# Kernel tuning notes

Hardware: AMD Instinct MI355X
Metric: run time of the kernel (lower is better)

The kernel has to match this reference:

```python
import jax, jax.numpy as jnp
import numpy as np
from jax import lax

B, DZ, H, U, T, V = 256, 512, 512, 16, 16, 512  # batch, latent, lstm hidden, segments, steps/segment, vocab


def setup_inputs() -> dict:
    key = jax.random.key(0)
    ks = jax.random.split(key, 32)
    w = lambda k, shape: jax.random.normal(k, shape, jnp.float32) * 0.05
    d = {
        'z': jax.random.normal(ks[0], (B, DZ), jnp.float32),
        'x': jax.random.randint(ks[1], (B, U * T), 0, V),
        # conductor init-state projection: DZ -> 4H
        'Wc': w(ks[2], (4 * H, DZ)), 'bc': jnp.zeros((4 * H,), jnp.float32),
        # conductor 2-layer LSTM (input H, hidden H)
        'cWih0': w(ks[3], (4 * H, H)), 'cWhh0': w(ks[4], (4 * H, H)),
        'cbih0': jnp.zeros((4 * H,), jnp.float32), 'cbhh0': jnp.zeros((4 * H,), jnp.float32),
        'cWih1': w(ks[5], (4 * H, H)), 'cWhh1': w(ks[6], (4 * H, H)),
        'cbih1': jnp.zeros((4 * H,), jnp.float32), 'cbhh1': jnp.zeros((4 * H,), jnp.float32),
        # decoder init-state projection: H -> 4H
        'Wd': w(ks[7], (4 * H, H)), 'bd': jnp.zeros((4 * H,), jnp.float32),
        # decoder 2-layer LSTM (layer0 input 2H, layer1 input H, hidden H)
        'dWih0': w(ks[8], (4 * H, 2 * H)), 'dWhh0': w(ks[9], (4 * H, H)),
        'dbih0': jnp.zeros((4 * H,), jnp.float32), 'dbhh0': jnp.zeros((4 * H,), jnp.float32),
        'dWih1': w(ks[10], (4 * H, H)), 'dWhh1': w(ks[11], (4 * H, H)),
        'dbih1': jnp.zeros((4 * H,), jnp.float32), 'dbhh1': jnp.zeros((4 * H,), jnp.float32),
        # token embedding and output distribution head
        'emb': w(ks[12], (V, H)),
        'Wo': w(ks[13], (V, H)), 'bo': jnp.zeros((V,), jnp.float32),
    }
    return d


def _cell(x, h, c, Wih, Whh, bih, bhh):
    # PyTorch LSTM gate order: i, f, g, o
    g = x @ Wih.T + bih + h @ Whh.T + bhh
    i, f, gg, o = jnp.split(g, 4, axis=-1)
    c = jax.nn.sigmoid(f) * c + jax.nn.sigmoid(i) * jnp.tanh(gg)
    h = jax.nn.sigmoid(o) * jnp.tanh(c)
    return h, c


def _lstm_layer(xp, h0, c0, Whh, bhh):
    # xp: [N, T, 4H] = precomputed x @ Wih.T + bih
    def step(carry, xg):
        h, c = carry
        g = xg + h @ Whh.T + bhh
        i, f, gg, o = jnp.split(g, 4, axis=-1)
        c = jax.nn.sigmoid(f) * c + jax.nn.sigmoid(i) * jnp.tanh(gg)
        h = jax.nn.sigmoid(o) * jnp.tanh(c)
        return (h, c), h
    _, ys = lax.scan(step, (h0, c0), jnp.swapaxes(xp, 0, 1))
    return jnp.swapaxes(ys, 0, 1)  # [N, T, H]


def reference(z, x, Wc, bc, cWih0, cWhh0, cbih0, cbhh0, cWih1, cWhh1, cbih1, cbhh1,
              Wd, bd, dWih0, dWhh0, dbih0, dbhh0, dWih1, dWhh1, dbih1, dbhh1,
              emb, Wo, bo):
    Bz = z.shape[0]
    # --- conductor ---
    ci = jnp.tanh(z @ Wc.T + bc)  # [B, 4H]
    h1, h2, c1, c2 = ci[:, :H], ci[:, H:2 * H], ci[:, 2 * H:3 * H], ci[:, 3 * H:]
    o0 = jnp.zeros((Bz, H), ci.dtype)

    def cstep(carry, _):
        o, h1, c1, h2, c2 = carry
        h1, c1 = _cell(o, h1, c1, cWih0, cWhh0, cbih0, cbhh0)
        h2, c2 = _cell(h1, h2, c2, cWih1, cWhh1, cbih1, cbhh1)
        return (h2, h1, c1, h2, c2), h2

    _, couts = lax.scan(cstep, (o0, h1, c1, h2, c2), None, length=U)
    cond_out = jnp.swapaxes(couts, 0, 1)  # [B, U, H]

    # --- decoder init states ---
    states = jnp.tanh(cond_out @ Wd.T + bd).reshape(Bz * U, 4 * H)
    dh1, dh2, dc1, dc2 = (states[:, :H], states[:, H:2 * H],
                          states[:, 2 * H:3 * H], states[:, 3 * H:])
    h_init = dh1 + dh2  # [BU, H]

    # --- teacher-forced decoder ---
    xt = x.reshape(Bz * U, T)
    e = emb[xt]  # [BU, T, H]
    e = jnp.concatenate([jnp.zeros((Bz * U, 1, H), e.dtype), e[:, :-1]], axis=1)
    inp = jnp.concatenate(
        [e, jnp.broadcast_to(h_init[:, None], (Bz * U, T, H))], axis=-1)  # [BU, T, 2H]

    y0 = _lstm_layer(inp @ dWih0.T + dbih0, dh1, dc1, dWhh0, dbhh0)
    y1 = _lstm_layer(y0 @ dWih1.T + dbih1, dh2, dc2, dWhh1, dbhh1)
    dist = jax.nn.softmax(y1 @ Wo.T + bo, axis=-1)  # [BU, T, V]
    return dist.reshape(Bz, U * T, V)
```

## Files before the change

kernel.cpp:

```cpp
#include <hip/hip_runtime.h>
#include <math.h>

#define AS1 __attribute__((address_space(1)))
#define AS3 __attribute__((address_space(3)))

typedef __attribute__((ext_vector_type(8))) short short8v;
typedef __attribute__((ext_vector_type(16))) float f32x16;

constexpr size_t PA4c = (size_t)4096 * 512;
constexpr size_t PABc = (size_t)256 * 512;

__device__ __forceinline__ float sigmoidf_(float x) { return 1.f / (1.f + expf(-x)); }
__device__ __forceinline__ unsigned int f2bfu(float f) {
    unsigned int u = __float_as_uint(f);
    return (u + 0x7FFF + ((u >> 16) & 1)) >> 16;
}
__device__ __forceinline__ float bf2f(unsigned int s) { return __uint_as_float(s << 16); }
__device__ __forceinline__ unsigned int pack2(float v) {
    unsigned int b0 = f2bfu(v);
    unsigned int b1 = f2bfu(v - bf2f(b0));
    return b0 | (b1 << 16);
}
__device__ __forceinline__ float unpack2(unsigned int p) { return bf2f(p & 0xffffu) + bf2f(p >> 16); }

__device__ __forceinline__ void xswz(int d, int ngx, int ngy, int& bx, int& by) {
    int nwg = ngx * ngy;
    int q = nwg >> 3, r = nwg & 7, xcd = d & 7, pos = d >> 3;
    int logical = (xcd < r ? xcd * (q + 1) : r * (q + 1) + (xcd - r) * q) + pos;
    bx = logical % ngx; by = logical / ngx;
}

template<int FM, int FN>
__device__ __forceinline__ void gemm_core(
    const short* __restrict__ A1, const short* __restrict__ B1,
    const short* __restrict__ A2, const short* __restrict__ B2,
    int M, int N, int nsteps, int pairSwitch,
    int bx, int by, short* lds, f32x16 (&acc)[FM][FN])
{
    constexpr int ABLK = 4 * FM, BBLK = 2 * FN;
    constexpr int ACH = 2 * ABLK * 2, BCH = 2 * BBLK * 2;
    constexpr int CHT = ACH + BCH;
    constexpr int CPW = CHT / 8;
    constexpr int NBUF = 3;
    constexpr int BUFSH = CHT * 512;
    const int tid = threadIdx.x, lane = tid & 63, wid = tid >> 6;
    const int wm = wid >> 1, wn = wid & 1;
    const int l31 = lane & 31, loct = lane >> 5;
    const int mblk0 = by * ABLK, nblk0 = bx * BBLK;
    const size_t planeA = (size_t)M * 512, planeB = (size_t)N * 512;

    const short* cur[CPW];
    const short* nxt[CPW];
    int ldo[CPW];
    #pragma unroll
    for (int i = 0; i < CPW; ++i) {
        int c = wid * CPW + i;
        ldo[i] = c * 512;
        size_t off;
        const short *b1, *b2;
        if (c < ACH) {
            int plane = c / (ABLK * 2), rem = c % (ABLK * 2), blk = rem >> 1, piece = rem & 1;
            off = (size_t)plane * planeA + (size_t)(mblk0 + blk) * 16384 + piece * 512 + lane * 8;
            b1 = A1; b2 = A2;
        } else {
            int cb = c - ACH;
            int plane = cb / (BBLK * 2), rem = cb % (BBLK * 2), blk = rem >> 1, piece = rem & 1;
            off = (size_t)plane * planeB + (size_t)(nblk0 + blk) * 16384 + piece * 512 + lane * 8;
            b1 = B1; b2 = B2;
        }
        cur[i] = b1 + off;
        nxt[i] = b2 ? (b2 + off) : (b1 + off);
    }

    #pragma unroll
    for (int fm = 0; fm < FM; ++fm)
        #pragma unroll
        for (int fn = 0; fn < FN; ++fn)
            acc[fm][fn] = (f32x16){};

    auto STAGE = [&](int bufIdx) {
        short* db = lds + bufIdx * BUFSH;
        #pragma unroll
        for (int i = 0; i < CPW; ++i) {
            __builtin_amdgcn_global_load_lds((const AS1 unsigned int*)cur[i],
                                             (AS3 unsigned int*)(db + ldo[i]), 16, 0, 0);
            cur[i] += 1024;
        }
    };

    STAGE(0); STAGE(1);
    asm volatile("s_waitcnt vmcnt(%0)" :: "n"(CPW) : "memory");
    __builtin_amdgcn_s_barrier();

    for (int t = 0; t < nsteps; ++t) {
        int s = t + NBUF - 1;
        if (s < nsteps) {
            if (s == pairSwitch) {
                #pragma unroll
                for (int i = 0; i < CPW; ++i) cur[i] = nxt[i];
            }
            STAGE(s % NBUF);
        }
        const short* L = lds + (t % NBUF) * BUFSH;
        #pragma unroll
        for (int ksub = 0; ksub < 2; ++ksub) {
            short8v a[FM][2], b[FN][2];
            #pragma unroll
            for (int p = 0; p < 2; ++p) {
                #pragma unroll
                for (int f = 0; f < FM; ++f)
                    a[f][p] = *(const short8v*)(L + (p * (ABLK * 2) + (wm * FM + f) * 2 + ksub) * 512
                                                  + loct * 256 + l31 * 8);
                #pragma unroll
                for (int f = 0; f < FN; ++f)
                    b[f][p] = *(const short8v*)(L + (ACH + p * (BBLK * 2) + (wn * FN + f) * 2 + ksub) * 512
                                                  + loct * 256 + l31 * 8);
            }
            #pragma unroll
            for (int pp = 0; pp < 3; ++pp) {
                const int pa = (pp == 2) ? 1 : 0, pb = (pp == 1) ? 1 : 0;
                #pragma unroll
                for (int fm = 0; fm < FM; ++fm)
                    #pragma unroll
                    for (int fn = 0; fn < FN; ++fn)
                        acc[fm][fn] = __builtin_amdgcn_mfma_f32_32x32x16_bf16(
                            a[fm][pa], b[fn][pb], acc[fm][fn], 0, 0, 0);
            }
        }
        if (t + 2 < nsteps)
            asm volatile("s_waitcnt vmcnt(%0) lgkmcnt(0)" :: "n"(CPW) : "memory");
        else
            asm volatile("s_waitcnt vmcnt(0) lgkmcnt(0)" ::: "memory");
        __builtin_amdgcn_s_barrier();
    }
}

template<int FM, int FN>
__device__ __forceinline__ void epi_f32(f32x16 (&acc)[FM][FN], int bx, int by, int N,
                                        float* __restrict__ Cout, const float* __restrict__ bias, int act)
{
    constexpr int ROWS = 128 * FM, COLS = 64 * FN;
    const int tid = threadIdx.x, lane = tid & 63, wid = tid >> 6;
    const int wm = wid >> 1, wn = wid & 1, l31 = lane & 31, loct = lane >> 5;
    #pragma unroll
    for (int fm = 0; fm < FM; ++fm)
        #pragma unroll
        for (int fn = 0; fn < FN; ++fn) {
            int col = bx * COLS + wn * FN * 32 + fn * 32 + l31;
            int rb  = by * ROWS + wm * FM * 32 + fm * 32 + 4 * loct;
            #pragma unroll
            for (int reg = 0; reg < 16; ++reg) {
                int row = rb + (reg & 3) + 8 * (reg >> 2);
                float xv = acc[fm][fn][reg] + (bias ? bias[row] : 0.f);
                if (act) xv = tanhf(xv);
                Cout[(size_t)row * N + col] = xv;
            }
        }
}

template<int FM, int FN>
__device__ __forceinline__ void epi_pack(f32x16 (&acc)[FM][FN], int bx, int by, int N,
                                         unsigned int* __restrict__ packOut)
{
    constexpr int ROWS = 128 * FM, COLS = 64 * FN;
    const int tid = threadIdx.x, lane = tid & 63, wid = tid >> 6;
    const int wm = wid >> 1, wn = wid & 1, l31 = lane & 31, loct = lane >> 5;
    uint4* P4 = (uint4*)packOut;
    #pragma unroll
    for (int fm = 0; fm < FM; ++fm)
        #pragma unroll
        for (int fn = 0; fn < FN; ++fn) {
            int col = bx * COLS + wn * FN * 32 + fn * 32 + l31;
            int ub = by * (ROWS / 4) + wm * FM * 8 + fm * 8 + loct;
            #pragma unroll
            for (int ug = 0; ug < 4; ++ug) {
                int u = ub + 2 * ug;
                uint4 v;
                v.x = pack2(acc[fm][fn][4 * ug + 0]);
                v.y = pack2(acc[fm][fn][4 * ug + 1]);
                v.z = pack2(acc[fm][fn][4 * ug + 2]);
                v.w = pack2(acc[fm][fn][4 * ug + 3]);
                P4[(size_t)u * N + col] = v;
            }
        }
}

template<int FM, int FN>
__device__ __forceinline__ void epi_gate(
    f32x16 (&acc)[FM][FN], int bx, int by, int N,
    short* lds, const float* __restrict__ bab,
    const unsigned int* __restrict__ hgP,
    const unsigned int* __restrict__ embT,
    const int* __restrict__ xidx,
    float* __restrict__ cT,
    short* __restrict__ hout, size_t hps,
    short* __restrict__ condp, size_t cps, int ustep)
{
    constexpr int ABLK = 4 * FM, BBLK = 2 * FN;
    constexpr int ROWS = 32 * ABLK, COLS = 32 * BBLK;
    constexpr int CHN = ABLK * BBLK * 256;
    const int tid = threadIdx.x, lane = tid & 63, wid = tid >> 6;
    const int wm = wid >> 1, wn = wid & 1, l31 = lane & 31, loct = lane >> 5;
    short* hl = lds;
    #pragma unroll
    for (int fm = 0; fm < FM; ++fm) {
        #pragma unroll
        for (int fn = 0; fn < FN; ++fn) {
            const int col = bx * COLS + wn * FN * 32 + fn * 32 + l31;
            const int tok = xidx ? xidx[(size_t)col * 16] : -1;
            const int ub = by * (ROWS / 4) + wm * FM * 8 + fm * 8 + loct;
            #pragma unroll
            for (int ug = 0; ug < 4; ++ug) {
                int u = ub + 2 * ug;
                float gi = acc[fm][fn][4 * ug + 0];
                float gf = acc[fm][fn][4 * ug + 1];
                float gg = acc[fm][fn][4 * ug + 2];
                float go = acc[fm][fn][4 * ug + 3];
                float4 bv = *(const float4*)&bab[4 * u];
                gi += bv.x; gf += bv.y; gg += bv.z; go += bv.w;
                if (hgP) {
                    uint4 hv = ((const uint4*)hgP)[(size_t)u * N + col];
                    gi += unpack2(hv.x); gf += unpack2(hv.y);
                    gg += unpack2(hv.z); go += unpack2(hv.w);
                }
                if (embT && tok >= 0) {
                    uint4 ev = ((const uint4*)embT)[(size_t)u * 512 + tok];
                    gi += unpack2(ev.x); gf += unpack2(ev.y);
                    gg += unpack2(ev.z); go += unpack2(ev.w);
                }
                size_t cidx = (size_t)u * N + col;
                float c = sigmoidf_(gf) * cT[cidx] + sigmoidf_(gi) * tanhf(gg);
                cT[cidx] = c;
                float h = sigmoidf_(go) * tanhf(c);
                unsigned int p01 = pack2(h);
                int u_loc = wm * FM * 8 + fm * 8 + loct + 2 * ug;
                int m_loc = wn * FN * 32 + fn * 32 + l31;
                int offl = ((m_loc >> 5) * ABLK + (u_loc >> 3)) * 256 + (m_loc & 31) * 8 + (u_loc & 7);
                hl[offl] = (short)(p01 & 0xffffu);
                hl[CHN + offl] = (short)(p01 >> 16);
                if (condp) {
                    int np = col * 16 + ustep;
                    size_t offc = ((size_t)((np >> 5) * 64 + (u >> 3))) * 256 + (np & 31) * 8 + (u & 7);
                    condp[offc] = (short)(p01 & 0xffffu);
                    condp[cps + offc] = (short)(p01 >> 16);
                }
            }
        }
    }
    __syncthreads();
    constexpr int LB = (ABLK == 8) ? 3 : 2;
    for (int p = 0; p < 2; ++p) {
        for (int jj = tid; jj < CHN / 8; jj += 512) {
            int lc = jj >> 5, m31 = jj & 31;
            int m5 = lc >> LB, u3 = lc & (ABLK - 1);
            size_t gc = (size_t)((bx * BBLK + m5) * 64 + by * ABLK + u3);
            *(short8v*)(hout + p * hps + gc * 256 + m31 * 8) = *(const short8v*)(hl + p * CHN + jj * 8);
        }
    }
}

template<int FM, int FN>
__global__ __launch_bounds__(512, 1) void gemm_f32k(
    const short* A1, const short* B1, const short* A2, const short* B2,
    int M, int N, int nsteps, int psw,
    float* Cout, const float* bias, int act)
{
    __shared__ __align__(16) short lds[3 * (2 * (4 * FM) * 2 + 2 * (2 * FN) * 2) * 512];
    int d = blockIdx.y * gridDim.x + blockIdx.x;
    int bx, by; xswz(d, gridDim.x, gridDim.y, bx, by);
    f32x16 acc[FM][FN];
    gemm_core<FM, FN>(A1, B1, A2, B2, M, N, nsteps, psw, bx, by, lds, acc);
    epi_f32<FM, FN>(acc, bx, by, N, Cout, bias, act);
}

template<int FM, int FN>
__global__ __launch_bounds__(512, 1) void gemm_packk(
    const short* A1, const short* B1, const short* A2, const short* B2,
    int M, int N, int nsteps, int psw, unsigned int* packOut)
{
    __shared__ __align__(16) short lds[3 * (2 * (4 * FM) * 2 + 2 * (2 * FN) * 2) * 512];
    int d = blockIdx.y * gridDim.x + blockIdx.x;
    int bx, by; xswz(d, gridDim.x, gridDim.y, bx, by);
    f32x16 acc[FM][FN];
    gemm_core<FM, FN>(A1, B1, A2, B2, M, N, nsteps, psw, bx, by, lds, acc);
    epi_pack<FM, FN>(acc, bx, by, N, packOut);
}

__device__ __forceinline__ void gbar(unsigned int* bar, unsigned int target)
{
    __syncthreads();
    if (threadIdx.x == 0) {
        __hip_atomic_fetch_add(bar, 1u, __ATOMIC_ACQ_REL, __HIP_MEMORY_SCOPE_AGENT);
        while (__hip_atomic_load(bar, __ATOMIC_ACQUIRE, __HIP_MEMORY_SCOPE_AGENT) < target)
            __builtin_amdgcn_s_sleep(2);
    }
    __syncthreads();
}

__global__ __launch_bounds__(512, 1) void cond_lstm(
    const short* cWih0P, const short* cWhh0P, const short* cWih1P, const short* cWhh1P,
    const float* babc0, const float* babc1,
    float* c1T, float* c2T,
    short* h1p0, short* h1p1, short* h2p0, short* h2p1,
    short* condp, unsigned int* bar)
{
    __shared__ __align__(16) short lds[3 * 12288];
    const int d = blockIdx.x;
    const int xcd = d & 7, j = d >> 3;
    const int by = xcd * 2 + (j & 1), bx = j >> 1;
    unsigned int gen = 0;
    for (int u = 0; u < 16; ++u) {
        const int pin = u & 1;
        short* h1in  = pin ? h1p1 : h1p0;  short* h1out = pin ? h1p0 : h1p1;
        short* h2in  = pin ? h2p1 : h2p0;  short* h2out = pin ? h2p0 : h2p1;
        {
            f32x16 acc[1][1];
            if (u == 0)
                gemm_core<1, 1>(cWhh0P, h1in, nullptr, nullptr, 2048, 256, 16, 100, bx, by, lds, acc);
            else
                gemm_core<1, 1>(cWih0P, h2in, cWhh0P, h1in, 2048, 256, 32, 16, bx, by, lds, acc);
            epi_gate<1, 1>(acc, bx, by, 256, lds, babc0, nullptr, nullptr, nullptr,
                           c1T, h1out, PABc, nullptr, 0, 0);
        }
        gbar(bar, (++gen) * 64);
        {
            f32x16 acc[1][1];
            gemm_core<1, 1>(cWih1P, h1out, cWhh1P, h2in, 2048, 256, 32, 16, bx, by, lds, acc);
            epi_gate<1, 1>(acc, bx, by, 256, lds, babc1, nullptr, nullptr, nullptr,
                           c2T, h2out, PABc, condp, PA4c, u);
        }
        gbar(bar, (++gen) * 64);
    }
}

__global__ __launch_bounds__(512, 1) void dec_k1(
    int doGate,
    const short* Ag, const short* Bg, const float* bab,
    const unsigned int* hgP, const unsigned int* embT, const int* xidx,
    float* cT, short* hout,
    const short* Aw, const short* Bw, float* Lout)
{
    __shared__ __align__(16) short lds[3 * 24576];
    const int dd = blockIdx.x;
    if (doGate) {
        int bx, by; xswz(dd, 32, 8, bx, by);
        f32x16 acc[2][2];
        gemm_core<2, 2>(Ag, Bg, nullptr, nullptr, 2048, 4096, 16, 100, bx, by, lds, acc);
        epi_gate<2, 2>(acc, bx, by, 4096, lds, bab, hgP, embT, xidx, cT, hout, PA4c, nullptr, 0, 0);
        __syncthreads();
    }
    if (Aw) {
        int bx, by; xswz(dd, 64, 4, bx, by);
        f32x16 acc[1][1];
        gemm_core<1, 1>(Aw, Bw, nullptr, nullptr, 512, 4096, 16, 100, bx, by, lds, acc);
        epi_f32<1, 1>(acc, bx, by, 4096, Lout, nullptr, 0);
    }
}

__global__ __launch_bounds__(512, 1) void dec_k2(
    int doGate,
    const short* A1, const short* B1, const short* A2, const short* B2,
    const float* bab, float* cT, short* hout,
    const float* Lsrc, const float* bo, float* outp, int tstep)
{
    __shared__ __align__(16) short lds[3 * 24576];
    const int dd = blockIdx.x;
    if (doGate) {
        int bx, by; xswz(dd, 32, 8, bx, by);
        f32x16 acc[2][2];
        gemm_core<2, 2>(A1, B1, A2, B2, 2048, 4096, 32, 16, bx, by, lds, acc);
        epi_gate<2, 2>(acc, bx, by, 4096, lds, bab, nullptr, nullptr, nullptr, cT, hout, PA4c, nullptr, 0, 0);
        __syncthreads();
    }
    if (Lsrc) {
        float* tile = (float*)lds;
        float* red  = (float*)lds + 16 * 513;
        float* red2 = red + 512;
        const int tid = threadIdx.x;
        const int mj = tid & 15, vs = tid >> 4;
        const int m = dd * 16 + mj;
        float mx = -1e30f;
        for (int i = 0; i < 16; ++i) {
            int v = vs * 16 + i;
            mx = fmaxf(mx, Lsrc[(size_t)v * 4096 + m] + bo[v]);
        }
        red[vs * 16 + mj] = mx;
        __syncthreads();
        for (int o = 16; o >= 1; o >>= 1) {
            if (vs < o) red[vs * 16 + mj] = fmaxf(red[vs * 16 + mj], red[(vs + o) * 16 + mj]);
            __syncthreads();
        }
        mx = red[mj];
        float sum = 0.f;
        for (int i = 0; i < 16; ++i) {
            int v = vs * 16 + i;
            float e = expf(Lsrc[(size_t)v * 4096 + m] + bo[v] - mx);
            sum += e;
            tile[mj * 513 + v] = e;
        }
        red2[vs * 16 + mj] = sum;
        __syncthreads();
        for (int o = 16; o >= 1; o >>= 1) {
            if (vs < o) red2[vs * 16 + mj] += red2[(vs + o) * 16 + mj];
            __syncthreads();
        }
        const int r = tid >> 5, c = tid & 31;
        float invr = 1.f / red2[r];
        for (int k = 0; k < 16; ++k) {
            int v = k * 32 + c;
            outp[((size_t)(dd * 16 + r) * 16 + tstep) * 512 + v] = tile[r * 513 + v] * invr;
        }
    }
}

struct PrepEnt { const float* src; const float* src2; void* dst; int ldw, col0, perm, total, op; };
struct PrepArgs { PrepEnt e[18]; int n; };

__global__ void prep_all(PrepArgs pa)
{
    for (int ei = 0; ei < pa.n; ++ei) {
        PrepEnt E = pa.e[ei];
        for (int o = blockIdx.x * 256 + threadIdx.x; o < E.total; o += gridDim.x * 256) {
            if (E.op == 0) {
                int c = o >> 8, w = o & 255, r = w >> 3, jj = w & 7;
                int n = (c >> 6) * 32 + r, k = (c & 63) * 8 + jj;
                int nsrc = E.perm ? ((n >> 2) + 512 * (n & 3)) : n;
                float v = E.src[(size_t)nsrc * E.ldw + E.col0 + k];
                unsigned int b0 = f2bfu(v);
                short* pl = (short*)E.dst;
                pl[o] = (short)b0;
                pl[E.total + o] = (short)f2bfu(v - bf2f(b0));
            } else {
                int src = (o >> 2) + 512 * (o & 3);
                ((float*)E.dst)[o] = E.src[src] + E.src2[src];
            }
        }
    }
}

__global__ void split_ci(const float* __restrict__ ciT, short* __restrict__ h1, short* __restrict__ h2,
                         size_t ps, float* __restrict__ c1T, float* __restrict__ c2T)
{
    int idx = blockIdx.x * 256 + threadIdx.x;
    int u = idx >> 8, b = idx & 255;
    float v1 = ciT[(size_t)u * 256 + b];
    float v2 = ciT[(size_t)(512 + u) * 256 + b];
    c1T[(size_t)u * 256 + b] = ciT[(size_t)(1024 + u) * 256 + b];
    c2T[(size_t)u * 256 + b] = ciT[(size_t)(1536 + u) * 256 + b];
    size_t o = ((size_t)((b >> 5) * 64 + (u >> 3))) * 256 + (b & 31) * 8 + (u & 7);
    unsigned int p;
    p = f2bfu(v1); h1[o] = (short)p; h1[ps + o] = (short)f2bfu(v1 - bf2f(p));
    p = f2bfu(v2); h2[o] = (short)p; h2[ps + o] = (short)f2bfu(v2 - bf2f(p));
}

__global__ void split_states(const float* __restrict__ GT, short* __restrict__ h0, short* __restrict__ h1d,
                             size_t ps, float* __restrict__ c0T, float* __restrict__ c1dT)
{
    int idx = blockIdx.x * 256 + threadIdx.x;
    int u = idx >> 12, m = idx & 4095;
    float a = GT[(size_t)u * 4096 + m];
    float b = GT[(size_t)(512 + u) * 4096 + m];
    c0T[(size_t)u * 4096 + m]  = GT[(size_t)(1024 + u) * 4096 + m];
    c1dT[(size_t)u * 4096 + m] = GT[(size_t)(1536 + u) * 4096 + m];
    size_t o = ((size_t)((m >> 5) * 64 + (u >> 3))) * 256 + (m & 31) * 8 + (u & 7);
    unsigned int p;
    p = f2bfu(a); h0[o] = (short)p; h0[ps + o] = (short)f2bfu(a - bf2f(p));
    p = f2bfu(b); h1d[o] = (short)p; h1d[ps + o] = (short)f2bfu(b - bf2f(p));
}

extern "C" void kernel_launch(void* const* d_in, const int* in_sizes, int n_in,
                              void* d_out, int out_size, void* d_ws, size_t ws_size,
                              hipStream_t stream)
{
    const float* z     = (const float*)d_in[0];
    const int*   x     = (const int*)  d_in[1];
    const float* Wc    = (const float*)d_in[2];
    const float* bc    = (const float*)d_in[3];
    const float* cWih0 = (const float*)d_in[4];
    const float* cWhh0 = (const float*)d_in[5];
    const float* cbih0 = (const float*)d_in[6];
    const float* cbhh0 = (const float*)d_in[7];
    const float* cWih1 = (const float*)d_in[8];
    const float* cWhh1 = (const float*)d_in[9];
    const float* cbih1 = (const float*)d_in[10];
    const float* cbhh1 = (const float*)d_in[11];
    const float* Wd    = (const float*)d_in[12];
    const float* bd    = (const float*)d_in[13];
    const float* dWih0 = (const float*)d_in[14];
    const float* dWhh0 = (const float*)d_in[15];
    const float* dbih0 = (const float*)d_in[16];
    const float* dbhh0 = (const float*)d_in[17];
    const float* dWih1 = (const float*)d_in[18];
    const float* dWhh1 = (const float*)d_in[19];
    const float* dbih1 = (const float*)d_in[20];
    const float* dbhh1 = (const float*)d_in[21];
    const float* emb   = (const float*)d_in[22];
    const float* Wo    = (const float*)d_in[23];
    const float* bo    = (const float*)d_in[24];
    float* out = (float*)d_out;
    (void)in_sizes; (void)n_in; (void)out_size; (void)ws_size;

    char* wsb = (char*)d_ws;
    size_t off = 0;
    auto alloc = [&](size_t bytes) -> void* {
        off = (off + 255) & ~(size_t)255;
        void* p = wsb + off;
        off += bytes;
        return p;
    };
    const size_t PW  = (size_t)2048 * 512;
    const size_t PWo = (size_t)512 * 512;

    short* WcP    = (short*)alloc(2 * PW * 2);
    short* WdP    = (short*)alloc(2 * PW * 2);
    short* dW1P   = (short*)alloc(2 * PW * 2);
    short* dW2P   = (short*)alloc(2 * PW * 2);
    short* cWih0P = (short*)alloc(2 * PW * 2);
    short* cWhh0P = (short*)alloc(2 * PW * 2);
    short* cWih1P = (short*)alloc(2 * PW * 2);
    short* cWhh1P = (short*)alloc(2 * PW * 2);
    short* dWhh0P = (short*)alloc(2 * PW * 2);
    short* dWih1P = (short*)alloc(2 * PW * 2);
    short* dWhh1P = (short*)alloc(2 * PW * 2);
    short* WoP    = (short*)alloc(2 * PWo * 2);
    short* zpl    = (short*)alloc(2 * PABc * 2);
    short* embpl  = (short*)alloc(2 * PWo * 2);
    float* babc0  = (float*)alloc(2048 * 4);
    float* babc1  = (float*)alloc(2048 * 4);
    float* babd0  = (float*)alloc(2048 * 4);
    float* babd1  = (float*)alloc(2048 * 4);
    float* GbufT  = (float*)alloc((size_t)2048 * 4096 * 4);
    unsigned int* hinitgP = (unsigned int*)alloc((size_t)512 * 4096 * 4 * 4);
    unsigned int* embW0P  = (unsigned int*)alloc((size_t)512 * 512 * 4 * 4);
    short* h1pl0 = (short*)alloc(2 * PABc * 2);
    short* h1pl1 = (short*)alloc(2 * PABc * 2);
    short* h2pl0 = (short*)alloc(2 * PABc * 2);
    short* h2pl1 = (short*)alloc(2 * PABc * 2);
    float* c1T = (float*)alloc((size_t)512 * 256 * 4);
    float* c2T = (float*)alloc((size_t)512 * 256 * 4);
    short* condpl = (short*)alloc(2 * PA4c * 2);
    short* h0pl[2];  short* h1dpl[2];
    h0pl[0]  = (short*)alloc(2 * PA4c * 2); h0pl[1]  = (short*)alloc(2 * PA4c * 2);
    h1dpl[0] = (short*)alloc(2 * PA4c * 2); h1dpl[1] = (short*)alloc(2 * PA4c * 2);
    float* c0T  = (float*)alloc((size_t)512 * 4096 * 4);
    float* c1dT = (float*)alloc((size_t)512 * 4096 * 4);
    unsigned int* bar = (unsigned int*)alloc(256);

    float* Lg[2] = { GbufT, GbufT + (size_t)512 * 4096 };

    PrepArgs pa; pa.n = 18;
    auto W8 = [](const float* s, void* d, int ldw, int col0, int perm, int total) {
        PrepEnt e; e.src = s; e.src2 = nullptr; e.dst = d; e.ldw = ldw; e.col0 = col0;
        e.perm = perm; e.total = total; e.op = 0; return e;
    };
    auto B8 = [](const float* a, const float* b, void* d) {
        PrepEnt e; e.src = a; e.src2 = b; e.dst = d; e.ldw = 0; e.col0 = 0;
        e.perm = 0; e.total = 2048; e.op = 1; return e;
    };
    pa.e[0]  = W8(Wc,    WcP,    512,  0,   0, 2048 * 512);
    pa.e[1]  = W8(Wd,    WdP,    512,  0,   0, 2048 * 512);
    pa.e[2]  = W8(dWih0, dW1P,   1024, 0,   1, 2048 * 512);
    pa.e[3]  = W8(dWih0, dW2P,   1024, 512, 1, 2048 * 512);
    pa.e[4]  = W8(cWih0, cWih0P, 512,  0,   1, 2048 * 512);
    pa.e[5]  = W8(cWhh0, cWhh0P, 512,  0,   1, 2048 * 512);
    pa.e[6]  = W8(cWih1, cWih1P, 512,  0,   1, 2048 * 512);
    pa.e[7]  = W8(cWhh1, cWhh1P, 512,  0,   1, 2048 * 512);
    pa.e[8]  = W8(dWhh0, dWhh0P, 512,  0,   1, 2048 * 512);
    pa.e[9]  = W8(dWih1, dWih1P, 512,  0,   1, 2048 * 512);
    pa.e[10] = W8(dWhh1, dWhh1P, 512,  0,   1, 2048 * 512);
    pa.e[11] = W8(Wo,    WoP,    512,  0,   0, 512 * 512);
    pa.e[12] = W8(z,     zpl,    512,  0,   0, 256 * 512);
    pa.e[13] = W8(emb,   embpl,  512,  0,   0, 512 * 512);
    pa.e[14] = B8(cbih0, cbhh0, babc0);
    pa.e[15] = B8(cbih1, cbhh1, babc1);
    pa.e[16] = B8(dbih0, dbhh0, babd0);
    pa.e[17] = B8(dbih1, dbhh1, babd1);
    prep_all<<<dim3(1024), dim3(256), 0, stream>>>(pa);
    hipMemsetAsync(bar, 0, 256, stream);

    gemm_f32k<2, 2><<<dim3(2, 8), dim3(512), 0, stream>>>(
        WcP, zpl, nullptr, nullptr, 2048, 256, 16, 100, GbufT, bc, 1);
    split_ci<<<dim3(512 * 256 / 256), dim3(256), 0, stream>>>(GbufT, h1pl0, h2pl0, PABc, c1T, c2T);

    gemm_packk<2, 2><<<dim3(4, 8), dim3(512), 0, stream>>>(
        dW1P, embpl, nullptr, nullptr, 2048, 512, 16, 100, embW0P);

    cond_lstm<<<dim3(64), dim3(512), 0, stream>>>(
        cWih0P, cWhh0P, cWih1P, cWhh1P, babc0, babc1,
        c1T, c2T, h1pl0, h1pl1, h2pl0, h2pl1, condpl, bar);

    gemm_f32k<2, 2><<<dim3(32, 8), dim3(512), 0, stream>>>(
        WdP, condpl, nullptr, nullptr, 2048, 4096, 16, 100, GbufT, bd, 1);
    split_states<<<dim3(512 * 4096 / 256), dim3(256), 0, stream>>>(
        GbufT, h0pl[0], h1dpl[0], PA4c, c0T, c1dT);

    gemm_packk<2, 2><<<dim3(32, 8), dim3(512), 0, stream>>>(
        dW2P, h0pl[0], dW2P, h1dpl[0], 2048, 4096, 32, 16, hinitgP);

    for (int t = 0; t < 16; ++t) {
        int pin = t & 1;
        dec_k1<<<dim3(256), dim3(512), 0, stream>>>(1,
            dWhh0P, h0pl[pin], babd0, hinitgP,
            t > 0 ? embW0P : nullptr, t > 0 ? x + (t - 1) : nullptr,
            c0T, h0pl[pin ^ 1],
            t > 0 ? WoP : nullptr, t > 0 ? h1dpl[pin] : nullptr,
            t > 0 ? Lg[(t - 1) & 1] : nullptr);
        dec_k2<<<dim3(256), dim3(512), 0, stream>>>(1,
            dWih1P, h0pl[pin ^ 1], dWhh1P, h1dpl[pin],
            babd1, c1dT, h1dpl[pin ^ 1],
            t > 0 ? Lg[(t - 1) & 1] : nullptr, bo, out, t - 1);
    }
    dec_k1<<<dim3(256), dim3(512), 0, stream>>>(0,
        nullptr, nullptr, nullptr, nullptr, nullptr, nullptr, nullptr, nullptr,
        WoP, h1dpl[0], Lg[1]);
    dec_k2<<<dim3(256), dim3(512), 0, stream>>>(0,
        nullptr, nullptr, nullptr, nullptr, nullptr, nullptr, nullptr,
        Lg[1], bo, out, 15);
}
```

Before: 2.690 ms.

## Split-K conductor LSTM across 256 blocks, fuse split kernels into GEMM epilogues

The conductor LSTM now runs on 256 blocks instead of 64. The K dimension is split four ways per tile, partial sums go through a global buffer with per-tile barriers, and each thread applies the gates element-wise. The init-state GEMMs now apply tanh and write packed h planes and c arrays directly, so the separate split_ci and split_states kernels are gone. The decoder gate epilogue batches its global loads ahead of the math, and the softmax keeps logits in registers so it no longer reads them twice. Together these aim to widen parallelism on the latency-bound serial conductor loop and cut launches and memory passes, at the cost of extra global round-trips and more grid-wide barriers per step.

```diff
diff --git a/kernel.cpp b/kernel.cpp
--- a/kernel.cpp
+++ b/kernel.cpp
@@ -30,12 +30,16 @@
     bx = logical % ngx; by = logical / ngx;
 }
 
+__device__ __forceinline__ size_t offf(int m, int k) {
+    return ((size_t)((m >> 5) * 64 + (k >> 3))) * 256 + (size_t)((m & 31) * 8 + (k & 7));
+}
+
 template<int FM, int FN>
 __device__ __forceinline__ void gemm_core(
     const short* __restrict__ A1, const short* __restrict__ B1,
     const short* __restrict__ A2, const short* __restrict__ B2,
     int M, int N, int nsteps, int pairSwitch,
-    int bx, int by, short* lds, f32x16 (&acc)[FM][FN])
+    int bx, int by, short* lds, f32x16 (&acc)[FM][FN], int koff)
 {
     constexpr int ABLK = 4 * FM, BBLK = 2 * FN;
     constexpr int ACH = 2 * ABLK * 2, BCH = 2 * BBLK * 2;
@@ -48,6 +52,7 @@
     const int l31 = lane & 31, loct = lane >> 5;
     const int mblk0 = by * ABLK, nblk0 = bx * BBLK;
     const size_t planeA = (size_t)M * 512, planeB = (size_t)N * 512;
+    const size_t koffs = (size_t)koff * 32;
 
     const short* cur[CPW];
     const short* nxt[CPW];
@@ -60,12 +65,12 @@
         const short *b1, *b2;
         if (c < ACH) {
             int plane = c / (ABLK * 2), rem = c % (ABLK * 2), blk = rem >> 1, piece = rem & 1;
-            off = (size_t)plane * planeA + (size_t)(mblk0 + blk) * 16384 + piece * 512 + lane * 8;
+            off = (size_t)plane * planeA + (size_t)(mblk0 + blk) * 16384 + piece * 512 + lane * 8 + koffs;
             b1 = A1; b2 = A2;
         } else {
             int cb = c - ACH;
             int plane = cb / (BBLK * 2), rem = cb % (BBLK * 2), blk = rem >> 1, piece = rem & 1;
-            off = (size_t)plane * planeB + (size_t)(nblk0 + blk) * 16384 + piece * 512 + lane * 8;
+            off = (size_t)plane * planeB + (size_t)(nblk0 + blk) * 16384 + piece * 512 + lane * 8 + koffs;
             b1 = B1; b2 = B2;
         }
         cur[i] = b1 + off;
@@ -186,51 +191,60 @@
 }
 
 template<int FM, int FN>
-__device__ __forceinline__ void epi_gate(
-    f32x16 (&acc)[FM][FN], int bx, int by, int N,
-    short* lds, const float* __restrict__ bab,
+__device__ __forceinline__ void epi_gate2(
+    f32x16 (&acc)[FM][FN], int bx, int by, int N, short* hl,
+    const float* __restrict__ bab,
     const unsigned int* __restrict__ hgP,
     const unsigned int* __restrict__ embT,
     const int* __restrict__ xidx,
     float* __restrict__ cT,
-    short* __restrict__ hout, size_t hps,
-    short* __restrict__ condp, size_t cps, int ustep)
+    short* __restrict__ hout, size_t hps)
 {
     constexpr int ABLK = 4 * FM, BBLK = 2 * FN;
     constexpr int ROWS = 32 * ABLK, COLS = 32 * BBLK;
     constexpr int CHN = ABLK * BBLK * 256;
     const int tid = threadIdx.x, lane = tid & 63, wid = tid >> 6;
     const int wm = wid >> 1, wn = wid & 1, l31 = lane & 31, loct = lane >> 5;
-    short* hl = lds;
     #pragma unroll
     for (int fm = 0; fm < FM; ++fm) {
         #pragma unroll
         for (int fn = 0; fn < FN; ++fn) {
             const int col = bx * COLS + wn * FN * 32 + fn * 32 + l31;
-            const int tok = xidx ? xidx[(size_t)col * 16] : -1;
             const int ub = by * (ROWS / 4) + wm * FM * 8 + fm * 8 + loct;
+            int tok = -1;
+            if (xidx) tok = xidx[(size_t)col * 16];
+            uint4 hv[4]; uint4 ev[4]; float cv[4]; float4 bv[4];
             #pragma unroll
             for (int ug = 0; ug < 4; ++ug) {
                 int u = ub + 2 * ug;
-                float gi = acc[fm][fn][4 * ug + 0];
-                float gf = acc[fm][fn][4 * ug + 1];
-                float gg = acc[fm][fn][4 * ug + 2];
-                float go = acc[fm][fn][4 * ug + 3];
-                float4 bv = *(const float4*)&bab[4 * u];
-                gi += bv.x; gf += bv.y; gg += bv.z; go += bv.w;
+                bv[ug] = *(const float4*)&bab[4 * u];
+                cv[ug] = cT[(size_t)u * N + col];
+                if (hgP) hv[ug] = ((const uint4*)hgP)[(size_t)u * N + col];
+            }
+            if (embT && tok >= 0) {
+                #pragma unroll
+                for (int ug = 0; ug < 4; ++ug) {
+                    int u = ub + 2 * ug;
+                    ev[ug] = ((const uint4*)embT)[(size_t)u * 512 + tok];
+                }
+            }
+            #pragma unroll
+            for (int ug = 0; ug < 4; ++ug) {
+                int u = ub + 2 * ug;
+                float gi = acc[fm][fn][4 * ug + 0] + bv[ug].x;
+                float gf = acc[fm][fn][4 * ug + 1] + bv[ug].y;
+                float gg = acc[fm][fn][4 * ug + 2] + bv[ug].z;
+                float go = acc[fm][fn][4 * ug + 3] + bv[ug].w;
                 if (hgP) {
-                    uint4 hv = ((const uint4*)hgP)[(size_t)u * N + col];
-                    gi += unpack2(hv.x); gf += unpack2(hv.y);
-                    gg += unpack2(hv.z); go += unpack2(hv.w);
+                    gi += unpack2(hv[ug].x); gf += unpack2(hv[ug].y);
+                    gg += unpack2(hv[ug].z); go += unpack2(hv[ug].w);
                 }
                 if (embT && tok >= 0) {
-                    uint4 ev = ((const uint4*)embT)[(size_t)u * 512 + tok];
-                    gi += unpack2(ev.x); gf += unpack2(ev.y);
-                    gg += unpack2(ev.z); go += unpack2(ev.w);
+                    gi += unpack2(ev[ug].x); gf += unpack2(ev[ug].y);
+                    gg += unpack2(ev[ug].z); go += unpack2(ev[ug].w);
                 }
-                size_t cidx = (size_t)u * N + col;
-                float c = sigmoidf_(gf) * cT[cidx] + sigmoidf_(gi) * tanhf(gg);
-                cT[cidx] = c;
+                float c = sigmoidf_(gf) * cv[ug] + sigmoidf_(gi) * tanhf(gg);
+                cT[(size_t)u * N + col] = c;
                 float h = sigmoidf_(go) * tanhf(c);
                 unsigned int p01 = pack2(h);
                 int u_loc = wm * FM * 8 + fm * 8 + loct + 2 * ug;
@@ -238,12 +252,6 @@
                 int offl = ((m_loc >> 5) * ABLK + (u_loc >> 3)) * 256 + (m_loc & 31) * 8 + (u_loc & 7);
                 hl[offl] = (short)(p01 & 0xffffu);
                 hl[CHN + offl] = (short)(p01 >> 16);
-                if (condp) {
-                    int np = col * 16 + ustep;
-                    size_t offc = ((size_t)((np >> 5) * 64 + (u >> 3))) * 256 + (np & 31) * 8 + (u & 7);
-                    condp[offc] = (short)(p01 & 0xffffu);
-                    condp[cps + offc] = (short)(p01 >> 16);
-                }
             }
         }
     }
@@ -259,77 +267,160 @@
     }
 }
 
+__device__ __forceinline__ void devbar(unsigned int* cnt, unsigned int target)
+{
+    __syncthreads();
+    if (threadIdx.x == 0) {
+        __hip_atomic_fetch_add(cnt, 1u, __ATOMIC_RELEASE, __HIP_MEMORY_SCOPE_AGENT);
+        while (__hip_atomic_load(cnt, __ATOMIC_RELAXED, __HIP_MEMORY_SCOPE_AGENT) < target)
+            __builtin_amdgcn_s_sleep(1);
+        unsigned int vv = __hip_atomic_load(cnt, __ATOMIC_ACQUIRE, __HIP_MEMORY_SCOPE_AGENT);
+        asm volatile("" :: "v"(vv));
+    }
+    __syncthreads();
+}
+
 template<int FM, int FN>
-__global__ __launch_bounds__(512, 1) void gemm_f32k(
+__global__ __launch_bounds__(512, 1) void gemm_packk(
     const short* A1, const short* B1, const short* A2, const short* B2,
-    int M, int N, int nsteps, int psw,
-    float* Cout, const float* bias, int act)
+    int M, int N, int nsteps, int psw, unsigned int* packOut)
 {
     __shared__ __align__(16) short lds[3 * (2 * (4 * FM) * 2 + 2 * (2 * FN) * 2) * 512];
     int d = blockIdx.y * gridDim.x + blockIdx.x;
     int bx, by; xswz(d, gridDim.x, gridDim.y, bx, by);
     f32x16 acc[FM][FN];
-    gemm_core<FM, FN>(A1, B1, A2, B2, M, N, nsteps, psw, bx, by, lds, acc);
-    epi_f32<FM, FN>(acc, bx, by, N, Cout, bias, act);
+    gemm_core<FM, FN>(A1, B1, A2, B2, M, N, nsteps, psw, bx, by, lds, acc, 0);
+    epi_pack<FM, FN>(acc, bx, by, N, packOut);
 }
 
 template<int FM, int FN>
-__global__ __launch_bounds__(512, 1) void gemm_packk(
-    const short* A1, const short* B1, const short* A2, const short* B2,
-    int M, int N, int nsteps, int psw, unsigned int* packOut)
+__global__ __launch_bounds__(512, 1) void gemm_split(
+    const short* A1, const short* B1, int M, int N, int nsteps,
+    const float* bias, short* hA, short* hB, size_t ps, float* cA, float* cB)
 {
     __shared__ __align__(16) short lds[3 * (2 * (4 * FM) * 2 + 2 * (2 * FN) * 2) * 512];
     int d = blockIdx.y * gridDim.x + blockIdx.x;
     int bx, by; xswz(d, gridDim.x, gridDim.y, bx, by);
     f32x16 acc[FM][FN];
-    gemm_core<FM, FN>(A1, B1, A2, B2, M, N, nsteps, psw, bx, by, lds, acc);
-    epi_pack<FM, FN>(acc, bx, by, N, packOut);
-}
-
-__device__ __forceinline__ void gbar(unsigned int* bar, unsigned int target)
-{
-    __syncthreads();
-    if (threadIdx.x == 0) {
-        __hip_atomic_fetch_add(bar, 1u, __ATOMIC_ACQ_REL, __HIP_MEMORY_SCOPE_AGENT);
-        while (__hip_atomic_load(bar, __ATOMIC_ACQUIRE, __HIP_MEMORY_SCOPE_AGENT) < target)
-            __builtin_amdgcn_s_sleep(2);
-    }
-    __syncthreads();
+    gemm_core<FM, FN>(A1, B1, nullptr, nullptr, M, N, nsteps, 100, bx, by, lds, acc, 0);
+    constexpr int ROWS = 128 * FM, COLS = 64 * FN;
+    const int tid = threadIdx.x, lane = tid & 63, wid = tid >> 6;
+    const int wm = wid >> 1, wn = wid & 1, l31 = lane & 31, loct = lane >> 5;
+    #pragma unroll
+    for (int fm = 0; fm < FM; ++fm)
+        #pragma unroll
+        for (int fn = 0; fn < FN; ++fn) {
+            int col = bx * COLS + wn * FN * 32 + fn * 32 + l31;
+            int rb  = by * ROWS + wm * FM * 32 + fm * 32 + 4 * loct;
+            #pragma unroll
+            for (int reg = 0; reg < 16; ++reg) {
+                int row = rb + (reg & 3) + 8 * (reg >> 2);
+                float xv = tanhf(acc[fm][fn][reg] + bias[row]);
+                if (row < 1024) {
+                    short* hp = (row < 512) ? hA : hB;
+                    size_t o = offf(col, row & 511);
+                    unsigned int p01 = pack2(xv);
+                    hp[o] = (short)(p01 & 0xffffu);
+                    hp[ps + o] = (short)(p01 >> 16);
+                } else {
+                    float* cp = (row < 1536) ? cA : cB;
+                    cp[(size_t)(row & 511) * N + col] = xv;
+                }
+            }
+        }
 }
 
 __global__ __launch_bounds__(512, 1) void cond_lstm(
     const short* cWih0P, const short* cWhh0P, const short* cWih1P, const short* cWhh1P,
     const float* babc0, const float* babc1,
-    float* c1T, float* c2T,
+    const float* c1T0, const float* c2T0,
     short* h1p0, short* h1p1, short* h2p0, short* h2p1,
-    short* condp, unsigned int* bar)
+    short* condp, float* P, unsigned int* bar, unsigned int* tbar)
 {
     __shared__ __align__(16) short lds[3 * 12288];
     const int d = blockIdx.x;
-    const int xcd = d & 7, j = d >> 3;
-    const int by = xcd * 2 + (j & 1), bx = j >> 1;
-    unsigned int gen = 0;
+    const int xcd = d & 7, slot = d >> 3;
+    const int by = xcd * 2 + (slot & 1);
+    const int bx = (slot >> 1) & 3;
+    const int ks = slot >> 3;
+    const int tileId = by * 4 + bx;
+    const int koff = (ks & 1) * 256;
+
+    const int lid = ks * 512 + threadIdx.x;
+    const int uf = by * 32 + (lid >> 6);
+    const int b  = bx * 64 + (lid & 63);
+    float c1 = c1T0[(size_t)uf * 256 + b];
+    float c2 = c2T0[(size_t)uf * 256 + b];
+
+    unsigned int gen = 0, tgen = 0;
     for (int u = 0; u < 16; ++u) {
         const int pin = u & 1;
-        short* h1in  = pin ? h1p1 : h1p0;  short* h1out = pin ? h1p0 : h1p1;
-        short* h2in  = pin ? h2p1 : h2p0;  short* h2out = pin ? h2p0 : h2p1;
+        const short* h1in = pin ? h1p1 : h1p0;  short* h1out = pin ? h1p0 : h1p1;
+        const short* h2in = pin ? h2p1 : h2p0;  short* h2out = pin ? h2p0 : h2p1;
+
         {
             f32x16 acc[1][1];
-            if (u == 0)
-                gemm_core<1, 1>(cWhh0P, h1in, nullptr, nullptr, 2048, 256, 16, 100, bx, by, lds, acc);
-            else
-                gemm_core<1, 1>(cWih0P, h2in, cWhh0P, h1in, 2048, 256, 32, 16, bx, by, lds, acc);
-            epi_gate<1, 1>(acc, bx, by, 256, lds, babc0, nullptr, nullptr, nullptr,
-                           c1T, h1out, PABc, nullptr, 0, 0);
-        }
-        gbar(bar, (++gen) * 64);
+            if (u == 0 && ks < 2) {
+                acc[0][0] = (f32x16){};
+            } else {
+                const short* A  = (ks < 2) ? cWih0P : cWhh0P;
+                const short* Bp = (ks < 2) ? h2in   : h1in;
+                gemm_core<1, 1>(A, Bp, nullptr, nullptr, 2048, 256, 8, 100, bx, by, lds, acc, koff);
+            }
+            epi_f32<1, 1>(acc, bx, by, 256, P + (size_t)ks * 524288, nullptr, 0);
+        }
+        devbar(tbar + tileId, (++tgen) * 4);
+        {
+            int k0 = (u == 0) ? 2 : 0;
+            float g[4];
+            #pragma unroll
+            for (int gg = 0; gg < 4; ++gg) {
+                int row = 4 * uf + gg;
+                float s[4];
+                for (int k4 = k0; k4 < 4; ++k4) s[k4] = P[(size_t)k4 * 524288 + (size_t)row * 256 + b];
+                float acc2 = babc0[row];
+                for (int k4 = k0; k4 < 4; ++k4) acc2 += s[k4];
+                g[gg] = acc2;
+            }
+            c1 = sigmoidf_(g[1]) * c1 + sigmoidf_(g[0]) * tanhf(g[2]);
+            float h = sigmoidf_(g[3]) * tanhf(c1);
+            unsigned int p01 = pack2(h);
+            size_t o = offf(b, uf);
+            h1out[o] = (short)(p01 & 0xffffu);
+            h1out[PABc + o] = (short)(p01 >> 16);
+        }
+        devbar(bar, (++gen) * 256);
         {
             f32x16 acc[1][1];
-            gemm_core<1, 1>(cWih1P, h1out, cWhh1P, h2in, 2048, 256, 32, 16, bx, by, lds, acc);
-            epi_gate<1, 1>(acc, bx, by, 256, lds, babc1, nullptr, nullptr, nullptr,
-                           c2T, h2out, PABc, condp, PA4c, u);
-        }
-        gbar(bar, (++gen) * 64);
+            const short* A  = (ks < 2) ? cWih1P : cWhh1P;
+            const short* Bp = (ks < 2) ? h1out  : h2in;
+            gemm_core<1, 1>(A, Bp, nullptr, nullptr, 2048, 256, 8, 100, bx, by, lds, acc, koff);
+            epi_f32<1, 1>(acc, bx, by, 256, P + (size_t)ks * 524288, nullptr, 0);
+        }
+        devbar(tbar + tileId, (++tgen) * 4);
+        {
+            float g[4];
+            #pragma unroll
+            for (int gg = 0; gg < 4; ++gg) {
+                int row = 4 * uf + gg;
+                float s0 = P[(size_t)0 * 524288 + (size_t)row * 256 + b];
+                float s1 = P[(size_t)1 * 524288 + (size_t)row * 256 + b];
+                float s2 = P[(size_t)2 * 524288 + (size_t)row * 256 + b];
+                float s3 = P[(size_t)3 * 524288 + (size_t)row * 256 + b];
+                g[gg] = babc1[row] + ((s0 + s1) + (s2 + s3));
+            }
+            c2 = sigmoidf_(g[1]) * c2 + sigmoidf_(g[0]) * tanhf(g[2]);
+            float h = sigmoidf_(g[3]) * tanhf(c2);
+            unsigned int p01 = pack2(h);
+            size_t o = offf(b, uf);
+            h2out[o] = (short)(p01 & 0xffffu);
+            h2out[PABc + o] = (short)(p01 >> 16);
+            int np = b * 16 + u;
+            size_t oc = offf(np, uf);
+            condp[oc] = (short)(p01 & 0xffffu);
+            condp[PA4c + oc] = (short)(p01 >> 16);
+        }
+        devbar(bar, (++gen) * 256);
     }
 }
 
@@ -345,14 +436,14 @@
     if (doGate) {
         int bx, by; xswz(dd, 32, 8, bx, by);
         f32x16 acc[2][2];
-        gemm_core<2, 2>(Ag, Bg, nullptr, nullptr, 2048, 4096, 16, 100, bx, by, lds, acc);
-        epi_gate<2, 2>(acc, bx, by, 4096, lds, bab, hgP, embT, xidx, cT, hout, PA4c, nullptr, 0, 0);
+        gemm_core<2, 2>(Ag, Bg, nullptr, nullptr, 2048, 4096, 16, 100, bx, by, lds, acc, 0);
+        epi_gate2<2, 2>(acc, bx, by, 4096, lds, bab, hgP, embT, xidx, cT, hout, PA4c);
         __syncthreads();
     }
     if (Aw) {
         int bx, by; xswz(dd, 64, 4, bx, by);
         f32x16 acc[1][1];
-        gemm_core<1, 1>(Aw, Bw, nullptr, nullptr, 512, 4096, 16, 100, bx, by, lds, acc);
+        gemm_core<1, 1>(Aw, Bw, nullptr, nullptr, 512, 4096, 16, 100, bx, by, lds, acc, 0);
         epi_f32<1, 1>(acc, bx, by, 4096, Lout, nullptr, 0);
     }
 }
@@ -368,8 +459,8 @@
     if (doGate) {
         int bx, by; xswz(dd, 32, 8, bx, by);
         f32x16 acc[2][2];
-        gemm_core<2, 2>(A1, B1, A2, B2, 2048, 4096, 32, 16, bx, by, lds, acc);
-        epi_gate<2, 2>(acc, bx, by, 4096, lds, bab, nullptr, nullptr, nullptr, cT, hout, PA4c, nullptr, 0, 0);
+        gemm_core<2, 2>(A1, B1, A2, B2, 2048, 4096, 32, 16, bx, by, lds, acc, 0);
+        epi_gate2<2, 2>(acc, bx, by, 4096, lds, bab, nullptr, nullptr, nullptr, cT, hout, PA4c);
         __syncthreads();
     }
     if (Lsrc) {
@@ -379,11 +470,15 @@
         const int tid = threadIdx.x;
         const int mj = tid & 15, vs = tid >> 4;
         const int m = dd * 16 + mj;
-        float mx = -1e30f;
+        float lv[16];
+        #pragma unroll
         for (int i = 0; i < 16; ++i) {
             int v = vs * 16 + i;
-            mx = fmaxf(mx, Lsrc[(size_t)v * 4096 + m] + bo[v]);
-        }
+            lv[i] = Lsrc[(size_t)v * 4096 + m] + bo[v];
+        }
+        float mx = lv[0];
+        #pragma unroll
+        for (int i = 1; i < 16; ++i) mx = fmaxf(mx, lv[i]);
         red[vs * 16 + mj] = mx;
         __syncthreads();
         for (int o = 16; o >= 1; o >>= 1) {
@@ -392,11 +487,11 @@
         }
         mx = red[mj];
         float sum = 0.f;
+        #pragma unroll
         for (int i = 0; i < 16; ++i) {
-            int v = vs * 16 + i;
-            float e = expf(Lsrc[(size_t)v * 4096 + m] + bo[v] - mx);
+            float e = expf(lv[i] - mx);
             sum += e;
-            tile[mj * 513 + v] = e;
+            tile[mj * 513 + vs * 16 + i] = e;
         }
         red2[vs * 16 + mj] = sum;
         __syncthreads();
@@ -436,36 +531,6 @@
             }
         }
     }
-}
-
-__global__ void split_ci(const float* __restrict__ ciT, short* __restrict__ h1, short* __restrict__ h2,
-                         size_t ps, float* __restrict__ c1T, float* __restrict__ c2T)
-{
-    int idx = blockIdx.x * 256 + threadIdx.x;
-    int u = idx >> 8, b = idx & 255;
-    float v1 = ciT[(size_t)u * 256 + b];
-    float v2 = ciT[(size_t)(512 + u) * 256 + b];
-    c1T[(size_t)u * 256 + b] = ciT[(size_t)(1024 + u) * 256 + b];
-    c2T[(size_t)u * 256 + b] = ciT[(size_t)(1536 + u) * 256 + b];
-    size_t o = ((size_t)((b >> 5) * 64 + (u >> 3))) * 256 + (b & 31) * 8 + (u & 7);
-    unsigned int p;
-    p = f2bfu(v1); h1[o] = (short)p; h1[ps + o] = (short)f2bfu(v1 - bf2f(p));
-    p = f2bfu(v2); h2[o] = (short)p; h2[ps + o] = (short)f2bfu(v2 - bf2f(p));
-}
-
-__global__ void split_states(const float* __restrict__ GT, short* __restrict__ h0, short* __restrict__ h1d,
-                             size_t ps, float* __restrict__ c0T, float* __restrict__ c1dT)
-{
-    int idx = blockIdx.x * 256 + threadIdx.x;
-    int u = idx >> 12, m = idx & 4095;
-    float a = GT[(size_t)u * 4096 + m];
-    float b = GT[(size_t)(512 + u) * 4096 + m];
-    c0T[(size_t)u * 4096 + m]  = GT[(size_t)(1024 + u) * 4096 + m];
-    c1dT[(size_t)u * 4096 + m] = GT[(size_t)(1536 + u) * 4096 + m];
-    size_t o = ((size_t)((m >> 5) * 64 + (u >> 3))) * 256 + (m & 31) * 8 + (u & 7);
-    unsigned int p;
-    p = f2bfu(a); h0[o] = (short)p; h0[ps + o] = (short)f2bfu(a - bf2f(p));
-    p = f2bfu(b); h1d[o] = (short)p; h1d[ps + o] = (short)f2bfu(b - bf2f(p));
 }
 
 extern "C" void kernel_launch(void* const* d_in, const int* in_sizes, int n_in,
@@ -544,8 +609,9 @@
     h1dpl[0] = (short*)alloc(2 * PA4c * 2); h1dpl[1] = (short*)alloc(2 * PA4c * 2);
     float* c0T  = (float*)alloc((size_t)512 * 4096 * 4);
     float* c1dT = (float*)alloc((size_t)512 * 4096 * 4);
-    unsigned int* bar = (unsigned int*)alloc(256);
-
+    unsigned int* barreg = (unsigned int*)alloc(512);
+
+    float* Pbuf  = GbufT;
     float* Lg[2] = { GbufT, GbufT + (size_t)512 * 4096 };
 
     PrepArgs pa; pa.n = 18;
@@ -576,23 +642,20 @@
     pa.e[16] = B8(dbih0, dbhh0, babd0);
     pa.e[17] = B8(dbih1, dbhh1, babd1);
     prep_all<<<dim3(1024), dim3(256), 0, stream>>>(pa);
-    hipMemsetAsync(bar, 0, 256, stream);
-
-    gemm_f32k<2, 2><<<dim3(2, 8), dim3(512), 0, stream>>>(
-        WcP, zpl, nullptr, nullptr, 2048, 256, 16, 100, GbufT, bc, 1);
-    split_ci<<<dim3(512 * 256 / 256), dim3(256), 0, stream>>>(GbufT, h1pl0, h2pl0, PABc, c1T, c2T);
+    hipMemsetAsync(barreg, 0, 512, stream);
+
+    gemm_split<2, 2><<<dim3(2, 8), dim3(512), 0, stream>>>(
+        WcP, zpl, 2048, 256, 16, bc, h1pl0, h2pl0, PABc, c1T, c2T);
 
     gemm_packk<2, 2><<<dim3(4, 8), dim3(512), 0, stream>>>(
         dW1P, embpl, nullptr, nullptr, 2048, 512, 16, 100, embW0P);
 
-    cond_lstm<<<dim3(64), dim3(512), 0, stream>>>(
-        cWih0P, cWhh0P, cWih1P, cWhh1P, babc0, babc1,
-        c1T, c2T, h1pl0, h1pl1, h2pl0, h2pl1, condpl, bar);
-
-    gemm_f32k<2, 2><<<dim3(32, 8), dim3(512), 0, stream>>>(
-        WdP, condpl, nullptr, nullptr, 2048, 4096, 16, 100, GbufT, bd, 1);
-    split_states<<<dim3(512 * 4096 / 256), dim3(256), 0, stream>>>(
-        GbufT, h0pl[0], h1dpl[0], PA4c, c0T, c1dT);
+    cond_lstm<<<dim3(256), dim3(512), 0, stream>>>(
+        cWih0P, cWhh0P, cWih1P, cWhh1P, babc0, babc1, c1T, c2T,
+        h1pl0, h1pl1, h2pl0, h2pl1, condpl, Pbuf, barreg, barreg + 16);
+
+    gemm_split<2, 2><<<dim3(32, 8), dim3(512), 0, stream>>>(
+        WdP, condpl, 2048, 4096, 16, bd, h0pl[0], h1dpl[0], PA4c, c0T, c1dT);
 
     gemm_packk<2, 2><<<dim3(32, 8), dim3(512), 0, stream>>>(
         dW2P, h0pl[0], dW2P, h1dpl[0], 2048, 4096, 32, 16, hinitgP);
```

Measured after the change: 3.018 ms. +12.2%, slower.
